# Optimization experiments

Measured on AMD Instinct MI355X. Metric: run time of the kernel, lower is better.

Reference implementation:

```python
import jax, jax.numpy as jnp
import numpy as np

N, E, F, H, G, EPS = 50000, 500000, 128, 192, 256, 1e-5


def setup_inputs() -> dict:
    key = jax.random.key(0)
    ks = jax.random.split(key, 16)
    s = 0.05
    return {
        "x": jax.random.normal(ks[0], (N, F), jnp.float32),
        "edge_index": jax.random.randint(ks[1], (2, E), 0, N),
        "batch": jnp.sort(jax.random.randint(ks[2], (N,), 0, G)),
        "num_graphs": G,
        "w_rel0": jax.random.normal(ks[3], (H, F)) * s,
        "b_rel0": jnp.zeros((H,), jnp.float32),
        "w_root0": jax.random.normal(ks[4], (H, F)) * s,
        "w_rel": jax.random.normal(ks[5], (3, H, H)) * s,
        "b_rel": jnp.zeros((3, H), jnp.float32),
        "w_root": jax.random.normal(ks[6], (3, H, H)) * s,
        "bn_gamma": jnp.ones((4, H), jnp.float32),
        "bn_beta": jnp.zeros((4, H), jnp.float32),
        "head_w1": jax.random.normal(ks[7], (H, H)) * s,
        "head_b1": jnp.zeros((H,), jnp.float32),
        "head_w2": jax.random.normal(ks[8], (H, H)) * s,
        "head_b2": jnp.zeros((H,), jnp.float32),
        "out_w": jax.random.normal(ks[9], (1, H)) * s,
        "out_b": jnpp if False else jnp.zeros((1,), jnp.float32),
    }


def _conv_bn_relu(x, src, dst, n_nodes, wr, br, wroot, gamma, beta):
    # PyG GraphConv: out_i = lin_rel(sum_{j->i} x_j) + lin_root(x_i)
    agg = jax.ops.segment_sum(x[src], dst, num_segments=n_nodes)  # [N, d]
    h = agg @ wr.T + br + x @ wroot.T                             # [N, H]
    mu = h.mean(axis=0)
    var = h.var(axis=0)  # biased, as torch BN train mode
    h = (h - mu) * jax.lax.rsqrt(var + EPS) * gamma + beta
    return jax.nn.relu(h)


def reference(x, edge_index, batch, num_graphs, w_rel0, b_rel0, w_root0,
              w_rel, b_rel, w_root, bn_gamma, bn_beta,
              head_w1, head_b1, head_w2, head_b2, out_w, out_b):
    src, dst = edge_index[0], edge_index[1]
    n_nodes = x.shape[0]
    h = _conv_bn_relu(x, src, dst, n_nodes, w_rel0, b_rel0, w_root0,
                      bn_gamma[0], bn_beta[0])
    for i in range(3):
        h = _conv_bn_relu(h, src, dst, n_nodes, w_rel[i], b_rel[i], w_root[i],
                          bn_gamma[i + 1], bn_beta[i + 1])
    # global mean pool per graph
    sums = jax.ops.segment_sum(h, batch, num_segments=num_graphs)   # [G, H]
    cnts = jax.ops.segment_sum(jnp.ones((n_nodes,), h.dtype), batch,
                               num_segments=num_graphs)
    g = sums / jnp.maximum(cnts, 1.0)[:, None]
    # MLP head (dropout = eval) + output linear
    hh = jax.nn.relu(g @ head_w1.T + head_b1) @ head_w2.T + head_b2
    out = hh @ out_w.T + out_b                                      # [G, 1]
    return out[:, 0]
```

## Files before the change

### kernel.cpp

```cpp
#include <hip/hip_runtime.h>

#define HD 192
#define FD0 128
#define NG 256
#define BNEPS 1e-5f

#define STAT_S  1048576.0f
#define STAT_IS (1.0f / 1048576.0f)
#define QS  2048.0f
#define QIS (1.0f / 2048.0f)
#define POOL_S  65536.0f
#define POOL_IS (1.0f / 65536.0f)

typedef unsigned short u16;
typedef __attribute__((ext_vector_type(8))) short bf16x8;
typedef __attribute__((ext_vector_type(4))) float f32x4;

static inline int idiv(int a, int b) { return (a + b - 1) / b; }

__device__ __forceinline__ float b2f(u16 u) {
    unsigned int v = ((unsigned int)u) << 16;
    return __builtin_bit_cast(float, v);
}
__device__ __forceinline__ u16 f2b(float f) {
    unsigned int x = __builtin_bit_cast(unsigned int, f);
    return (u16)((x + 0x7FFFu + ((x >> 16) & 1u)) >> 16);
}
__device__ __forceinline__ short f2q(float v) {
    return (short)__float2int_rn(fmaxf(fminf(v, 15.9f), -15.9f) * QS);
}

__device__ __forceinline__ void async_cp16(const void* g, void* l) {
    __builtin_amdgcn_global_load_lds(
        (const __attribute__((address_space(1))) unsigned int*)g,
        (__attribute__((address_space(3))) unsigned int*)l, 16, 0, 0);
}

__global__ __launch_bounds__(256) void convert_x(const float* __restrict__ in,
    u16* __restrict__ xb, short* __restrict__ xq, int n4)
{
    const int i = blockIdx.x * 256 + threadIdx.x;
    if (i >= n4) return;
    const float4 v = ((const float4*)in)[i];
    u16 o[4] = { f2b(v.x), f2b(v.y), f2b(v.z), f2b(v.w) };
    ((ushort4*)xb)[i] = *(ushort4*)o;
    short q[4] = { f2q(v.x), f2q(v.y), f2q(v.z), f2q(v.w) };
    ((short4*)xq)[i] = *(short4*)q;
}

__device__ __forceinline__ void pack_one(const float* __restrict__ wr,
    const float* __restrict__ wt, u16* __restrict__ out, int K, int idx)
{
    const int j  = idx & 7;
    const int t  = idx >> 3;
    const int c  = t & 15;
    const int kg = (t >> 4) & 3;
    const int rest = t >> 6;
    const int fglob = rest % 12;
    const int chunk = rest / 12;
    const int col = fglob * 16 + c;
    const int k   = chunk * 32 + kg * 8 + j;
    const float v = (k < K) ? wr[(size_t)col * K + k] : wt[(size_t)col * K + (k - K)];
    out[idx] = f2b(v);
}

__global__ __launch_bounds__(256) void pack_all(const float* __restrict__ wr0,
    const float* __restrict__ wt0, const float* __restrict__ w_rel,
    const float* __restrict__ w_root, u16* __restrict__ wp0,
    u16* __restrict__ wp123)
{
    const int T0 = HD * 2 * FD0;
    const int T1 = HD * 2 * HD;
    int idx = blockIdx.x * 256 + threadIdx.x;
    if (idx < T0) {
        pack_one(wr0, wt0, wp0, FD0, idx);
    } else {
        idx -= T0;
        if (idx >= 3 * T1) return;
        const int li = idx / T1;
        const int r  = idx - li * T1;
        pack_one(w_rel + (size_t)li * HD * HD, w_root + (size_t)li * HD * HD,
                 wp123 + (size_t)li * T1, HD, r);
    }
}

__global__ __launch_bounds__(256) void transpose_all(const float* __restrict__ w1,
    const float* __restrict__ w2, float* __restrict__ w1t, float* __restrict__ w2t)
{
    int idx = blockIdx.x * 256 + threadIdx.x;
    const float* w = w1; float* o = w1t;
    if (idx >= HD * HD) { idx -= HD * HD; w = w2; o = w2t; }
    if (idx >= HD * HD) return;
    const int t = idx % HD, k = idx / HD;
    o[idx] = w[(size_t)t * HD + k];
}

__global__ __launch_bounds__(256) void hist_kernel(const int* __restrict__ dst,
                                                   int* __restrict__ deg, int E)
{
    const int e = blockIdx.x * 256 + threadIdx.x;
    if (e < E) atomicAdd(&deg[dst[e]], 1);
}

__global__ __launch_bounds__(256) void scan_partial(const int* __restrict__ deg,
                                                    int* __restrict__ psum, int N)
{
    __shared__ int s[256];
    const int t = threadIdx.x;
    const int i = blockIdx.x * 256 + t;
    s[t] = (i < N) ? deg[i] : 0;
    __syncthreads();
    for (int off = 128; off > 0; off >>= 1) {
        if (t < off) s[t] += s[t + off];
        __syncthreads();
    }
    if (t == 0) psum[blockIdx.x] = s[0];
}

__global__ __launch_bounds__(256) void scan_small(int* __restrict__ psum, int M)
{
    __shared__ int s[256];
    const int t = threadIdx.x;
    s[t] = (t < M) ? psum[t] : 0;
    __syncthreads();
    for (int off = 1; off < 256; off <<= 1) {
        const int u = (t >= off) ? s[t - off] : 0;
        __syncthreads();
        s[t] += u;
        __syncthreads();
    }
    if (t < M) psum[t] = (t == 0) ? 0 : s[t - 1];
}

__global__ __launch_bounds__(256) void scan_expand(const int* __restrict__ deg,
    const int* __restrict__ psum, int* __restrict__ rowptr, int N, int E)
{
    __shared__ int s[256];
    const int t = threadIdx.x;
    const int i = blockIdx.x * 256 + t;
    const int v = (i < N) ? deg[i] : 0;
    s[t] = v;
    __syncthreads();
    for (int off = 1; off < 256; off <<= 1) {
        const int u = (t >= off) ? s[t - off] : 0;
        __syncthreads();
        s[t] += u;
        __syncthreads();
    }
    if (i < N) rowptr[i] = psum[blockIdx.x] + s[t] - v;
    if (i == N - 1) rowptr[N] = E;
}

__global__ __launch_bounds__(256) void fill_kernel(const int* __restrict__ src,
    const int* __restrict__ dst, const int* __restrict__ rowptr,
    int* __restrict__ cursor, int* __restrict__ eidx, int E)
{
    const int e = blockIdx.x * 256 + threadIdx.x;
    if (e >= E) return;
    const int d = dst[e];
    const int p = atomicAdd(&cursor[d], 1);
    eidx[rowptr[d] + p] = src[e];
}

template<int FD>
__global__ __launch_bounds__(256) void gather_kernel(
    const short* __restrict__ hq, const int* __restrict__ rowptr,
    const int* __restrict__ eidx, u16* __restrict__ aggb, int N)
{
    constexpr int GW = FD / 32;
    constexpr int ND = GW / 2;
    const int lane = threadIdx.x & 63;
    const int half = lane >> 5;
    const int g    = lane & 31;
    const int n    = blockIdx.x * 4 + (threadIdx.x >> 6);
    if (n >= N) return;
    const int beg = rowptr[n], end = rowptr[n + 1];

    int acc[GW];
#pragma unroll
    for (int i = 0; i < GW; ++i) acc[i] = 0;

    int j = beg + half;
    for (; j + 6 < end; j += 8) {
        const int s0 = eidx[j],     s1 = eidx[j + 2];
        const int s2 = eidx[j + 4], s3 = eidx[j + 6];
        const unsigned int* p0 = (const unsigned int*)(hq + (size_t)s0 * FD + g * GW);
        const unsigned int* p1 = (const unsigned int*)(hq + (size_t)s1 * FD + g * GW);
        const unsigned int* p2 = (const unsigned int*)(hq + (size_t)s2 * FD + g * GW);
        const unsigned int* p3 = (const unsigned int*)(hq + (size_t)s3 * FD + g * GW);
        unsigned int u0[ND], u1[ND], u2[ND], u3[ND];
#pragma unroll
        for (int d = 0; d < ND; ++d) { u0[d] = p0[d]; u1[d] = p1[d]; u2[d] = p2[d]; u3[d] = p3[d]; }
#pragma unroll
        for (int d = 0; d < ND; ++d) {
            acc[2*d]   += (int)(short)(u0[d] & 0xffffu) + (int)(short)(u1[d] & 0xffffu)
                        + (int)(short)(u2[d] & 0xffffu) + (int)(short)(u3[d] & 0xffffu);
            acc[2*d+1] += (((int)u0[d]) >> 16) + (((int)u1[d]) >> 16)
                        + (((int)u2[d]) >> 16) + (((int)u3[d]) >> 16);
        }
    }
    for (; j < end; j += 2) {
        const int s0 = eidx[j];
        const unsigned int* p0 = (const unsigned int*)(hq + (size_t)s0 * FD + g * GW);
#pragma unroll
        for (int d = 0; d < ND; ++d) {
            const unsigned int u = p0[d];
            acc[2*d]   += (int)(short)(u & 0xffffu);
            acc[2*d+1] += ((int)u) >> 16;
        }
    }
#pragma unroll
    for (int i = 0; i < GW; ++i) acc[i] += __shfl_xor(acc[i], 32);

    if (half == 0) {
        unsigned int* q = (unsigned int*)(aggb + (size_t)n * FD + g * GW);
#pragma unroll
        for (int d = 0; d < ND; ++d) {
            const u16 lo = f2b((float)acc[2*d]   * QIS);
            const u16 hi = f2b((float)acc[2*d+1] * QIS);
            q[d] = (unsigned int)lo | ((unsigned int)hi << 16);
        }
    }
}

template<int K1, int K2>
__global__ __launch_bounds__(512, 1) void gemm_mfma(
    const u16* __restrict__ A1, const u16* __restrict__ A2,
    const u16* __restrict__ Wb, const float* __restrict__ bias,
    u16* __restrict__ Hout, long long* __restrict__ statsq, int N)
{
    constexpr int KC  = K1 + K2;
    constexpr int NC  = KC / 32;
    constexpr int NC1 = K1 / 32;
    __shared__ u16 bsh[HD * KC];

    const int tid  = threadIdx.x;
    const int wave = tid >> 6, lane = tid & 63;
    const int c = lane & 15, kg = lane >> 4;
    const int row0 = blockIdx.x * 256 + wave * 32;

    {
        constexpr int NST = (HD * KC) / (512 * 8);
        const u16* wsrc = Wb + tid * 8;
        u16* ldst = bsh + tid * 8;
#pragma unroll
        for (int i = 0; i < NST; ++i)
            async_cp16(wsrc + i * 4096, ldst + i * 4096);
    }

    int arc[2];
#pragma unroll
    for (int m = 0; m < 2; ++m) {
        const int r = row0 + m * 16 + c;
        arc[m] = r < N ? r : N - 1;
    }

    f32x4 acc[2][12];
#pragma unroll
    for (int m = 0; m < 2; ++m)
#pragma unroll
        for (int f = 0; f < 12; ++f) acc[m][f] = (f32x4){0.f, 0.f, 0.f, 0.f};

    __syncthreads();

    for (int ch = 0; ch < NC; ++ch) {
        const int kk = ch * 32;
        bf16x8 a[2];
#pragma unroll
        for (int m = 0; m < 2; ++m) {
            const u16* p = (ch < NC1) ? (A1 + (size_t)arc[m] * K1 + kk + kg * 8)
                                      : (A2 + (size_t)arc[m] * K2 + (kk - K1) + kg * 8);
            a[m] = *(const bf16x8*)p;
        }
#pragma unroll
        for (int f = 0; f < 12; ++f) {
            const bf16x8 b = *(const bf16x8*)&bsh[ch * 6144 + f * 512 + kg * 128 + c * 8];
            acc[0][f] = __builtin_amdgcn_mfma_f32_16x16x32_bf16(a[0], b, acc[0][f], 0, 0, 0);
            acc[1][f] = __builtin_amdgcn_mfma_f32_16x16x32_bf16(a[1], b, acc[1][f], 0, 0, 0);
        }
    }

    float s1v[12], s2v[12];
#pragma unroll
    for (int f = 0; f < 12; ++f) { s1v[f] = 0.f; s2v[f] = 0.f; }

#pragma unroll
    for (int f = 0; f < 12; ++f) {
        const int col = f * 16 + c;
        const float bv = bias[col];
#pragma unroll
        for (int m = 0; m < 2; ++m)
#pragma unroll
            for (int r = 0; r < 4; ++r) {
                const int orow = row0 + m * 16 + kg * 4 + r;
                if (orow < N) {
                    const float v = acc[m][f][r] + bv;
                    s1v[f] += v;
                    s2v[f] += v * v;
                    Hout[(size_t)orow * HD + col] = f2b(v);
                }
            }
    }
#pragma unroll
    for (int f = 0; f < 12; ++f) {
        s1v[f] += __shfl_xor(s1v[f], 16); s1v[f] += __shfl_xor(s1v[f], 32);
        s2v[f] += __shfl_xor(s2v[f], 16); s2v[f] += __shfl_xor(s2v[f], 32);
    }
    __syncthreads();
    float* red = (float*)bsh;
    if (kg == 0) {
#pragma unroll
        for (int f = 0; f < 12; ++f) {
            red[wave * HD + f * 16 + c]            = s1v[f];
            red[8 * HD + wave * HD + f * 16 + c]   = s2v[f];
        }
    }
    __syncthreads();
    if (tid < HD) {
        float a1 = 0.f, a2 = 0.f;
#pragma unroll
        for (int w = 0; w < 8; ++w) {
            a1 += red[w * HD + tid];
            a2 += red[8 * HD + w * HD + tid];
        }
        atomicAdd((unsigned long long*)&statsq[tid],
                  (unsigned long long)(long long)llrintf(a1 * STAT_S));
        atomicAdd((unsigned long long*)&statsq[HD + tid],
                  (unsigned long long)(long long)llrintf(a2 * STAT_S));
    }
}

__global__ __launch_bounds__(256) void norm_relu(const u16* __restrict__ hpre,
    u16* __restrict__ hb, short* __restrict__ hq,
    const long long* __restrict__ statsq,
    const float* __restrict__ gamma, const float* __restrict__ beta, int N)
{
    __shared__ float sc[HD], sh[HD];
    const int t = threadIdx.x;
    if (t < HD) {
        const float inv = 1.0f / (float)N;
        const float sum = (float)statsq[t] * STAT_IS;
        const float sq  = (float)statsq[HD + t] * STAT_IS;
        const float mu  = sum * inv;
        const float var = sq * inv - mu * mu;
        const float s   = gamma[t] * rsqrtf(var + BNEPS);
        sc[t] = s; sh[t] = beta[t] - mu * s;
    }
    __syncthreads();
    const int idx = blockIdx.x * 256 + t;
    const int total = N * (HD / 8);
    if (idx >= total) return;
    const int c8 = idx % (HD / 8);
    uint4 packed = ((const uint4*)hpre)[idx];
    const u16* pu = (const u16*)&packed;
    u16 ob[8]; short oq[8];
#pragma unroll
    for (int j = 0; j < 8; ++j) {
        const int cc = c8 * 8 + j;
        const float v = fmaxf(0.f, fmaf(b2f(pu[j]), sc[cc], sh[cc]));
        ob[j] = f2b(v);
        oq[j] = (short)__float2int_rn(fminf(v, 15.9f) * QS);
    }
    ((uint4*)hb)[idx] = *(uint4*)ob;
    ((uint4*)hq)[idx] = *(uint4*)oq;
}

__global__ __launch_bounds__(192) void pool_partial(const u16* __restrict__ hb,
    const int* __restrict__ batch, int* __restrict__ gsumq, int N)
{
    const int t   = threadIdx.x;
    const int rl  = t / 24;
    const int oct = t % 24;
    const int r0  = blockIdx.x * 256;
    const int rend = (r0 + 256 < N) ? r0 + 256 : N;

    float facc[8];
#pragma unroll
    for (int i = 0; i < 8; ++i) facc[i] = 0.f;
    int cur = -1;

    for (int r = r0 + rl; r < rend; r += 8) {
        const int b = batch[r];
        if (b != cur) {
            if (cur >= 0) {
                int* q = gsumq + (size_t)cur * HD + oct * 8;
#pragma unroll
                for (int i = 0; i < 8; ++i)
                    atomicAdd(&q[i], __float2int_rn(facc[i] * POOL_S));
            }
#pragma unroll
            for (int i = 0; i < 8; ++i) facc[i] = 0.f;
            cur = b;
        }
        const uint4 pv = *(const uint4*)(hb + (size_t)r * HD + oct * 8);
        const u16* pu = (const u16*)&pv;
#pragma unroll
        for (int i = 0; i < 8; ++i) facc[i] += b2f(pu[i]);
    }
    if (cur >= 0) {
        int* q = gsumq + (size_t)cur * HD + oct * 8;
#pragma unroll
        for (int i = 0; i < 8; ++i)
            atomicAdd(&q[i], __float2int_rn(facc[i] * POOL_S));
    }
}

__global__ __launch_bounds__(192) void head_kernel(
    const int* __restrict__ gsumq, const int* __restrict__ batch, int N,
    const float* __restrict__ w1t, const float* __restrict__ b1,
    const float* __restrict__ w2t, const float* __restrict__ b2,
    const float* __restrict__ ow, const float* __restrict__ ob,
    float* __restrict__ out)
{
    __shared__ float gv[HD];
    __shared__ float h1[HD];
    __shared__ float h2[HD];
    const int g = blockIdx.x;
    const int t = threadIdx.x;

    int lo = 0, hi = N;
    while (lo < hi) { int m = (lo + hi) >> 1; if (batch[m] < g) lo = m + 1; else hi = m; }
    const int start = lo;
    hi = N;
    while (lo < hi) { int m = (lo + hi) >> 1; if (batch[m] < g + 1) lo = m + 1; else hi = m; }
    const int end = lo;
    const float cnt = fmaxf((float)(end - start), 1.0f);

    gv[t] = (float)gsumq[(size_t)g * HD + t] * POOL_IS / cnt;
    __syncthreads();
    {
        float acc = b1[t];
#pragma unroll 4
        for (int k = 0; k < HD; ++k)
            acc = fmaf(gv[k], w1t[k * HD + t], acc);
        h1[t] = fmaxf(acc, 0.f);
    }
    __syncthreads();
    {
        float acc = b2[t];
#pragma unroll 4
        for (int k = 0; k < HD; ++k)
            acc = fmaf(h1[k], w2t[k * HD + t], acc);
        h2[t] = acc * ow[t];
    }
    __syncthreads();
    if (t < 64) {
        float s = h2[t] + h2[t + 64] + h2[t + 128];
#pragma unroll
        for (int d = 1; d < 64; d <<= 1) s += __shfl_xor(s, d);
        if (t == 0) out[g] = s + ob[0];
    }
}

extern "C" void kernel_launch(void* const* d_in, const int* in_sizes, int n_in,
                              void* d_out, int out_size, void* d_ws, size_t ws_size,
                              hipStream_t stream)
{
    const float* x       = (const float*)d_in[0];
    const int*   ei      = (const int*)d_in[1];
    const int*   batch   = (const int*)d_in[2];
    const float* w_rel0  = (const float*)d_in[4];
    const float* b_rel0  = (const float*)d_in[5];
    const float* w_root0 = (const float*)d_in[6];
    const float* w_rel   = (const float*)d_in[7];
    const float* b_rel   = (const float*)d_in[8];
    const float* w_root  = (const float*)d_in[9];
    const float* bn_g    = (const float*)d_in[10];
    const float* bn_b    = (const float*)d_in[11];
    const float* hw1     = (const float*)d_in[12];
    const float* hb1     = (const float*)d_in[13];
    const float* hw2     = (const float*)d_in[14];
    const float* hb2     = (const float*)d_in[15];
    const float* ow      = (const float*)d_in[16];
    const float* ob      = (const float*)d_in[17];
    float* out = (float*)d_out;

    const int N = in_sizes[0] / FD0;
    const int E = in_sizes[1] / 2;
    const int* src = ei;
    const int* dst = ei + E;
    const int M = idiv(N, 256);

    char* ws = (char*)d_ws;
    size_t off = 0;
    u16*   xb   = (u16*)(ws + off);   off += (size_t)N * FD0 * 2;
    short* xq   = (short*)(ws + off); off += (size_t)N * FD0 * 2;
    u16*   hb   = (u16*)(ws + off);   off += (size_t)N * HD * 2;
    short* hq   = (short*)(ws + off); off += (size_t)N * HD * 2;
    u16*   aggb = (u16*)(ws + off);   off += (size_t)N * HD * 2;
    u16*   hpre = (u16*)(ws + off);   off += (size_t)N * HD * 2;
    u16*   wp0  = (u16*)(ws + off);   off += (size_t)HD * 2 * FD0 * 2;
    u16*   wp123= (u16*)(ws + off);   off += (size_t)3 * HD * 2 * HD * 2;
    off = (off + 15) & ~(size_t)15;
    float* w1t = (float*)(ws + off); off += (size_t)HD * HD * 4;
    float* w2t = (float*)(ws + off); off += (size_t)HD * HD * 4;
    long long* statsq4 = (long long*)(ws + off); off += 4 * 2 * HD * sizeof(long long);
    int*   gsumq  = (int*)(ws + off); off += (size_t)NG * HD * 4;
    int*   rowptr = (int*)(ws + off); off += (size_t)(N + 1) * 4;
    int*   deg    = (int*)(ws + off); off += (size_t)N * 4;
    int*   psum   = (int*)(ws + off); off += (size_t)M * 4;
    int*   eidx   = (int*)(ws + off); off += (size_t)E * 4;

    const dim3 b256(256), b512(512), b192(192);

    convert_x<<<idiv(N * FD0 / 4, 256), b256, 0, stream>>>(x, xb, xq, N * FD0 / 4);
    pack_all<<<idiv(HD * 2 * FD0 + 3 * HD * 2 * HD, 256), b256, 0, stream>>>(
        w_rel0, w_root0, w_rel, w_root, wp0, wp123);
    transpose_all<<<idiv(2 * HD * HD, 256), b256, 0, stream>>>(hw1, hw2, w1t, w2t);
    hipMemsetAsync(statsq4, 0, 4 * 2 * HD * sizeof(long long) + (size_t)NG * HD * 4,
                   stream);
    hipMemsetAsync(deg, 0, (size_t)N * sizeof(int), stream);
    hist_kernel<<<idiv(E, 256), b256, 0, stream>>>(dst, deg, E);
    scan_partial<<<M, b256, 0, stream>>>(deg, psum, N);
    scan_small<<<1, b256, 0, stream>>>(psum, M);
    scan_expand<<<M, b256, 0, stream>>>(deg, psum, rowptr, N, E);
    hipMemsetAsync(deg, 0, (size_t)N * sizeof(int), stream);
    fill_kernel<<<idiv(E, 256), b256, 0, stream>>>(src, dst, rowptr, deg, eidx, E);

    gather_kernel<FD0><<<idiv(N, 4), b256, 0, stream>>>(xq, rowptr, eidx, aggb, N);
    gemm_mfma<FD0, FD0><<<idiv(N, 256), b512, 0, stream>>>(aggb, xb, wp0, b_rel0,
                                                           hpre, statsq4, N);
    norm_relu<<<idiv(N * (HD / 8), 256), b256, 0, stream>>>(hpre, hb, hq, statsq4,
                                                            bn_g, bn_b, N);

    for (int i = 0; i < 3; ++i) {
        long long* statsq = statsq4 + (size_t)(i + 1) * 2 * HD;
        gather_kernel<HD><<<idiv(N, 4), b256, 0, stream>>>(hq, rowptr, eidx, aggb, N);
        gemm_mfma<HD, HD><<<idiv(N, 256), b512, 0, stream>>>(
            aggb, hb, wp123 + (size_t)i * HD * 2 * HD,
            b_rel + (size_t)i * HD, hpre, statsq, N);
        norm_relu<<<idiv(N * (HD / 8), 256), b256, 0, stream>>>(hpre, hb, hq, statsq,
            bn_g + (size_t)(i + 1) * HD, bn_b + (size_t)(i + 1) * HD, N);
    }

    pool_partial<<<idiv(N, 256), b192, 0, stream>>>(hb, batch, gsumq, N);
    head_kernel<<<NG, b192, 0, stream>>>(gsumq, batch, N, w1t, hb1, w2t, hb2,
                                         ow, ob, out);
}
```

Before: 418.6 us.

## Gather from bf16 features directly, drop int16 copies, fuse setup kernels, prefetch A

Removes the separate int16 quantized feature arrays (xq, hq), so the gather reads the bf16 activations and sums them in fp32, and norm_relu/convert no longer write a second copy. Merges the head-weight transpose into the packing kernel. The scan now writes absolute row offsets into the cursor, which removes a memset and the rowptr lookup in fill. Adds register double-buffering of A-operand loads in the MFMA GEMM. These cut write traffic and launch count, at the cost of fp32 accumulation instead of integer adds, which changes the numerics slightly and makes the sum order-dependent.

Measured after the change: 405.8 us. -3.1%, faster.

```diff
diff --git a/kernel.cpp b/kernel.cpp
--- a/kernel.cpp
+++ b/kernel.cpp
@@ -7,8 +7,6 @@
 
 #define STAT_S  1048576.0f
 #define STAT_IS (1.0f / 1048576.0f)
-#define QS  2048.0f
-#define QIS (1.0f / 2048.0f)
 #define POOL_S  65536.0f
 #define POOL_IS (1.0f / 65536.0f)
 
@@ -22,12 +20,15 @@
     unsigned int v = ((unsigned int)u) << 16;
     return __builtin_bit_cast(float, v);
 }
+__device__ __forceinline__ float b2f_lo(unsigned int u) {
+    return __builtin_bit_cast(float, u << 16);
+}
+__device__ __forceinline__ float b2f_hi(unsigned int u) {
+    return __builtin_bit_cast(float, u & 0xffff0000u);
+}
 __device__ __forceinline__ u16 f2b(float f) {
     unsigned int x = __builtin_bit_cast(unsigned int, f);
     return (u16)((x + 0x7FFFu + ((x >> 16) & 1u)) >> 16);
-}
-__device__ __forceinline__ short f2q(float v) {
-    return (short)__float2int_rn(fmaxf(fminf(v, 15.9f), -15.9f) * QS);
 }
 
 __device__ __forceinline__ void async_cp16(const void* g, void* l) {
@@ -36,16 +37,14 @@
         (__attribute__((address_space(3))) unsigned int*)l, 16, 0, 0);
 }
 
-__global__ __launch_bounds__(256) void convert_x(const float* __restrict__ in,
-    u16* __restrict__ xb, short* __restrict__ xq, int n4)
+__global__ __launch_bounds__(256) void convert_bf16(const float* __restrict__ in,
+                                                    u16* __restrict__ out, int n4)
 {
     const int i = blockIdx.x * 256 + threadIdx.x;
     if (i >= n4) return;
     const float4 v = ((const float4*)in)[i];
     u16 o[4] = { f2b(v.x), f2b(v.y), f2b(v.z), f2b(v.w) };
-    ((ushort4*)xb)[i] = *(ushort4*)o;
-    short q[4] = { f2q(v.x), f2q(v.y), f2q(v.z), f2q(v.w) };
-    ((short4*)xq)[i] = *(short4*)q;
+    ((ushort4*)out)[i] = *(ushort4*)o;
 }
 
 __device__ __forceinline__ void pack_one(const float* __restrict__ wr,
@@ -64,35 +63,32 @@
     out[idx] = f2b(v);
 }
 
-__global__ __launch_bounds__(256) void pack_all(const float* __restrict__ wr0,
+__global__ __launch_bounds__(256) void pack_fuse(const float* __restrict__ wr0,
     const float* __restrict__ wt0, const float* __restrict__ w_rel,
-    const float* __restrict__ w_root, u16* __restrict__ wp0,
-    u16* __restrict__ wp123)
+    const float* __restrict__ w_root, const float* __restrict__ hw1,
+    const float* __restrict__ hw2, u16* __restrict__ wp0,
+    u16* __restrict__ wp123, float* __restrict__ w1t, float* __restrict__ w2t)
 {
     const int T0 = HD * 2 * FD0;
     const int T1 = HD * 2 * HD;
+    const int TW = HD * HD;
     int idx = blockIdx.x * 256 + threadIdx.x;
-    if (idx < T0) {
-        pack_one(wr0, wt0, wp0, FD0, idx);
-    } else {
-        idx -= T0;
-        if (idx >= 3 * T1) return;
+    if (idx < T0) { pack_one(wr0, wt0, wp0, FD0, idx); return; }
+    idx -= T0;
+    if (idx < 3 * T1) {
         const int li = idx / T1;
         const int r  = idx - li * T1;
         pack_one(w_rel + (size_t)li * HD * HD, w_root + (size_t)li * HD * HD,
                  wp123 + (size_t)li * T1, HD, r);
-    }
-}
-
-__global__ __launch_bounds__(256) void transpose_all(const float* __restrict__ w1,
-    const float* __restrict__ w2, float* __restrict__ w1t, float* __restrict__ w2t)
-{
-    int idx = blockIdx.x * 256 + threadIdx.x;
-    const float* w = w1; float* o = w1t;
-    if (idx >= HD * HD) { idx -= HD * HD; w = w2; o = w2t; }
-    if (idx >= HD * HD) return;
-    const int t = idx % HD, k = idx / HD;
-    o[idx] = w[(size_t)t * HD + k];
+        return;
+    }
+    idx -= 3 * T1;
+    if (idx >= 2 * TW) return;
+    const float* w = (idx < TW) ? hw1 : hw2;
+    float*       o = (idx < TW) ? w1t : w2t;
+    const int r = (idx < TW) ? idx : idx - TW;
+    const int t = r % HD, k = r / HD;
+    o[r] = w[(size_t)t * HD + k];
 }
 
 __global__ __launch_bounds__(256) void hist_kernel(const int* __restrict__ dst,
@@ -132,7 +128,7 @@
     if (t < M) psum[t] = (t == 0) ? 0 : s[t - 1];
 }
 
-__global__ __launch_bounds__(256) void scan_expand(const int* __restrict__ deg,
+__global__ __launch_bounds__(256) void scan_expand(int* __restrict__ deg,
     const int* __restrict__ psum, int* __restrict__ rowptr, int N, int E)
 {
     __shared__ int s[256];
@@ -147,24 +143,27 @@
         s[t] += u;
         __syncthreads();
     }
-    if (i < N) rowptr[i] = psum[blockIdx.x] + s[t] - v;
+    if (i < N) {
+        const int base = psum[blockIdx.x] + s[t] - v;
+        rowptr[i] = base;
+        deg[i]    = base;
+    }
     if (i == N - 1) rowptr[N] = E;
 }
 
 __global__ __launch_bounds__(256) void fill_kernel(const int* __restrict__ src,
-    const int* __restrict__ dst, const int* __restrict__ rowptr,
-    int* __restrict__ cursor, int* __restrict__ eidx, int E)
+    const int* __restrict__ dst, int* __restrict__ cursor,
+    int* __restrict__ eidx, int E)
 {
     const int e = blockIdx.x * 256 + threadIdx.x;
     if (e >= E) return;
-    const int d = dst[e];
-    const int p = atomicAdd(&cursor[d], 1);
-    eidx[rowptr[d] + p] = src[e];
+    const int p = atomicAdd(&cursor[dst[e]], 1);
+    eidx[p] = src[e];
 }
 
 template<int FD>
 __global__ __launch_bounds__(256) void gather_kernel(
-    const short* __restrict__ hq, const int* __restrict__ rowptr,
+    const u16* __restrict__ hb, const int* __restrict__ rowptr,
     const int* __restrict__ eidx, u16* __restrict__ aggb, int N)
 {
     constexpr int GW = FD / 32;
@@ -176,37 +175,35 @@
     if (n >= N) return;
     const int beg = rowptr[n], end = rowptr[n + 1];
 
-    int acc[GW];
-#pragma unroll
-    for (int i = 0; i < GW; ++i) acc[i] = 0;
+    float acc[GW];
+#pragma unroll
+    for (int i = 0; i < GW; ++i) acc[i] = 0.f;
 
     int j = beg + half;
     for (; j + 6 < end; j += 8) {
         const int s0 = eidx[j],     s1 = eidx[j + 2];
         const int s2 = eidx[j + 4], s3 = eidx[j + 6];
-        const unsigned int* p0 = (const unsigned int*)(hq + (size_t)s0 * FD + g * GW);
-        const unsigned int* p1 = (const unsigned int*)(hq + (size_t)s1 * FD + g * GW);
-        const unsigned int* p2 = (const unsigned int*)(hq + (size_t)s2 * FD + g * GW);
-        const unsigned int* p3 = (const unsigned int*)(hq + (size_t)s3 * FD + g * GW);
+        const unsigned int* p0 = (const unsigned int*)(hb + (size_t)s0 * FD + g * GW);
+        const unsigned int* p1 = (const unsigned int*)(hb + (size_t)s1 * FD + g * GW);
+        const unsigned int* p2 = (const unsigned int*)(hb + (size_t)s2 * FD + g * GW);
+        const unsigned int* p3 = (const unsigned int*)(hb + (size_t)s3 * FD + g * GW);
         unsigned int u0[ND], u1[ND], u2[ND], u3[ND];
 #pragma unroll
         for (int d = 0; d < ND; ++d) { u0[d] = p0[d]; u1[d] = p1[d]; u2[d] = p2[d]; u3[d] = p3[d]; }
 #pragma unroll
         for (int d = 0; d < ND; ++d) {
-            acc[2*d]   += (int)(short)(u0[d] & 0xffffu) + (int)(short)(u1[d] & 0xffffu)
-                        + (int)(short)(u2[d] & 0xffffu) + (int)(short)(u3[d] & 0xffffu);
-            acc[2*d+1] += (((int)u0[d]) >> 16) + (((int)u1[d]) >> 16)
-                        + (((int)u2[d]) >> 16) + (((int)u3[d]) >> 16);
+            acc[2*d]   += b2f_lo(u0[d]) + b2f_lo(u1[d]) + b2f_lo(u2[d]) + b2f_lo(u3[d]);
+            acc[2*d+1] += b2f_hi(u0[d]) + b2f_hi(u1[d]) + b2f_hi(u2[d]) + b2f_hi(u3[d]);
         }
     }
     for (; j < end; j += 2) {
         const int s0 = eidx[j];
-        const unsigned int* p0 = (const unsigned int*)(hq + (size_t)s0 * FD + g * GW);
+        const unsigned int* p0 = (const unsigned int*)(hb + (size_t)s0 * FD + g * GW);
 #pragma unroll
         for (int d = 0; d < ND; ++d) {
             const unsigned int u = p0[d];
-            acc[2*d]   += (int)(short)(u & 0xffffu);
-            acc[2*d+1] += ((int)u) >> 16;
+            acc[2*d]   += b2f_lo(u);
+            acc[2*d+1] += b2f_hi(u);
         }
     }
 #pragma unroll
@@ -216,8 +213,8 @@
         unsigned int* q = (unsigned int*)(aggb + (size_t)n * FD + g * GW);
 #pragma unroll
         for (int d = 0; d < ND; ++d) {
-            const u16 lo = f2b((float)acc[2*d]   * QIS);
-            const u16 hi = f2b((float)acc[2*d+1] * QIS);
+            const u16 lo = f2b(acc[2*d]);
+            const u16 hi = f2b(acc[2*d+1]);
             q[d] = (unsigned int)lo | ((unsigned int)hi << 16);
         }
     }
@@ -261,23 +258,30 @@
 #pragma unroll
         for (int f = 0; f < 12; ++f) acc[m][f] = (f32x4){0.f, 0.f, 0.f, 0.f};
 
-    __syncthreads();
-
+    auto aload = [&](int ch, bf16x8* d) {
+#pragma unroll
+        for (int m = 0; m < 2; ++m) {
+            const u16* p = (ch < NC1)
+                ? (A1 + (size_t)arc[m] * K1 + ch * 32 + kg * 8)
+                : (A2 + (size_t)arc[m] * K2 + (ch - NC1) * 32 + kg * 8);
+            d[m] = *(const bf16x8*)p;
+        }
+    };
+
+    bf16x8 a_cur[2], a_nxt[2];
+    aload(0, a_cur);
+    __syncthreads();
+
+#pragma unroll
     for (int ch = 0; ch < NC; ++ch) {
-        const int kk = ch * 32;
-        bf16x8 a[2];
-#pragma unroll
-        for (int m = 0; m < 2; ++m) {
-            const u16* p = (ch < NC1) ? (A1 + (size_t)arc[m] * K1 + kk + kg * 8)
-                                      : (A2 + (size_t)arc[m] * K2 + (kk - K1) + kg * 8);
-            a[m] = *(const bf16x8*)p;
-        }
+        if (ch + 1 < NC) aload(ch + 1, a_nxt);
 #pragma unroll
         for (int f = 0; f < 12; ++f) {
             const bf16x8 b = *(const bf16x8*)&bsh[ch * 6144 + f * 512 + kg * 128 + c * 8];
-            acc[0][f] = __builtin_amdgcn_mfma_f32_16x16x32_bf16(a[0], b, acc[0][f], 0, 0, 0);
-            acc[1][f] = __builtin_amdgcn_mfma_f32_16x16x32_bf16(a[1], b, acc[1][f], 0, 0, 0);
-        }
+            acc[0][f] = __builtin_amdgcn_mfma_f32_16x16x32_bf16(a_cur[0], b, acc[0][f], 0, 0, 0);
+            acc[1][f] = __builtin_amdgcn_mfma_f32_16x16x32_bf16(a_cur[1], b, acc[1][f], 0, 0, 0);
+        }
+        a_cur[0] = a_nxt[0]; a_cur[1] = a_nxt[1];
     }
 
     float s1v[12], s2v[12];
@@ -331,8 +335,7 @@
 }
 
 __global__ __launch_bounds__(256) void norm_relu(const u16* __restrict__ hpre,
-    u16* __restrict__ hb, short* __restrict__ hq,
-    const long long* __restrict__ statsq,
+    u16* __restrict__ hb, const long long* __restrict__ statsq,
     const float* __restrict__ gamma, const float* __restrict__ beta, int N)
 {
     __shared__ float sc[HD], sh[HD];
@@ -353,16 +356,13 @@
     const int c8 = idx % (HD / 8);
     uint4 packed = ((const uint4*)hpre)[idx];
     const u16* pu = (const u16*)&packed;
-    u16 ob[8]; short oq[8];
+    u16 ob[8];
 #pragma unroll
     for (int j = 0; j < 8; ++j) {
         const int cc = c8 * 8 + j;
-        const float v = fmaxf(0.f, fmaf(b2f(pu[j]), sc[cc], sh[cc]));
-        ob[j] = f2b(v);
-        oq[j] = (short)__float2int_rn(fminf(v, 15.9f) * QS);
+        ob[j] = f2b(fmaxf(0.f, fmaf(b2f(pu[j]), sc[cc], sh[cc])));
     }
     ((uint4*)hb)[idx] = *(uint4*)ob;
-    ((uint4*)hq)[idx] = *(uint4*)oq;
 }
 
 __global__ __launch_bounds__(192) void pool_partial(const u16* __restrict__ hb,
@@ -484,9 +484,7 @@
     char* ws = (char*)d_ws;
     size_t off = 0;
     u16*   xb   = (u16*)(ws + off);   off += (size_t)N * FD0 * 2;
-    short* xq   = (short*)(ws + off); off += (size_t)N * FD0 * 2;
     u16*   hb   = (u16*)(ws + off);   off += (size_t)N * HD * 2;
-    short* hq   = (short*)(ws + off); off += (size_t)N * HD * 2;
     u16*   aggb = (u16*)(ws + off);   off += (size_t)N * HD * 2;
     u16*   hpre = (u16*)(ws + off);   off += (size_t)N * HD * 2;
     u16*   wp0  = (u16*)(ws + off);   off += (size_t)HD * 2 * FD0 * 2;
@@ -503,10 +501,10 @@
 
     const dim3 b256(256), b512(512), b192(192);
 
-    convert_x<<<idiv(N * FD0 / 4, 256), b256, 0, stream>>>(x, xb, xq, N * FD0 / 4);
-    pack_all<<<idiv(HD * 2 * FD0 + 3 * HD * 2 * HD, 256), b256, 0, stream>>>(
-        w_rel0, w_root0, w_rel, w_root, wp0, wp123);
-    transpose_all<<<idiv(2 * HD * HD, 256), b256, 0, stream>>>(hw1, hw2, w1t, w2t);
+    convert_bf16<<<idiv(N * FD0 / 4, 256), b256, 0, stream>>>(x, xb, N * FD0 / 4);
+    pack_fuse<<<idiv(HD * 2 * FD0 + 3 * HD * 2 * HD + 2 * HD * HD, 256), b256, 0,
+                stream>>>(w_rel0, w_root0, w_rel, w_root, hw1, hw2,
+                          wp0, wp123, w1t, w2t);
     hipMemsetAsync(statsq4, 0, 4 * 2 * HD * sizeof(long long) + (size_t)NG * HD * 4,
                    stream);
     hipMemsetAsync(deg, 0, (size_t)N * sizeof(int), stream);
@@ -514,22 +512,21 @@
     scan_partial<<<M, b256, 0, stream>>>(deg, psum, N);
     scan_small<<<1, b256, 0, stream>>>(psum, M);
     scan_expand<<<M, b256, 0, stream>>>(deg, psum, rowptr, N, E);
-    hipMemsetAsync(deg, 0, (size_t)N * sizeof(int), stream);
-    fill_kernel<<<idiv(E, 256), b256, 0, stream>>>(src, dst, rowptr, deg, eidx, E);
-
-    gather_kernel<FD0><<<idiv(N, 4), b256, 0, stream>>>(xq, rowptr, eidx, aggb, N);
+    fill_kernel<<<idiv(E, 256), b256, 0, stream>>>(src, dst, deg, eidx, E);
+
+    gather_kernel<FD0><<<idiv(N, 4), b256, 0, stream>>>(xb, rowptr, eidx, aggb, N);
     gemm_mfma<FD0, FD0><<<idiv(N, 256), b512, 0, stream>>>(aggb, xb, wp0, b_rel0,
                                                            hpre, statsq4, N);
-    norm_relu<<<idiv(N * (HD / 8), 256), b256, 0, stream>>>(hpre, hb, hq, statsq4,
+    norm_relu<<<idiv(N * (HD / 8), 256), b256, 0, stream>>>(hpre, hb, statsq4,
                                                             bn_g, bn_b, N);
 
     for (int i = 0; i < 3; ++i) {
         long long* statsq = statsq4 + (size_t)(i + 1) * 2 * HD;
-        gather_kernel<HD><<<idiv(N, 4), b256, 0, stream>>>(hq, rowptr, eidx, aggb, N);
+        gather_kernel<HD><<<idiv(N, 4), b256, 0, stream>>>(hb, rowptr, eidx, aggb, N);
         gemm_mfma<HD, HD><<<idiv(N, 256), b512, 0, stream>>>(
             aggb, hb, wp123 + (size_t)i * HD * 2 * HD,
             b_rel + (size_t)i * HD, hpre, statsq, N);
-        norm_relu<<<idiv(N * (HD / 8), 256), b256, 0, stream>>>(hpre, hb, hq, statsq,
+        norm_relu<<<idiv(N * (HD / 8), 256), b256, 0, stream>>>(hpre, hb, statsq,
             bn_g + (size_t)(i + 1) * HD, bn_b + (size_t)(i + 1) * HD, N);
     }
 
```
